# Kernel optimization log

Measured on AMD Instinct MI355X. Metric: run time of the kernel, lower is better.

Reference implementation:

```python
import math
import jax, jax.numpy as jnp
import numpy as np

N, T, F, H = 30000, 4, 128, 8  # num_node, num_type, num_fea, num_head
D = F // H


def setup_inputs() -> dict:
    key = jax.random.key(0)
    k0, k1, k2, k3, k4 = jax.random.split(key, 5)
    feature = jax.random.normal(k0, (N, F), dtype=jnp.float32)
    edge_fea = jax.random.normal(k1, (N, T, F), dtype=jnp.float32)
    node_multi_mask = jax.random.randint(k2, (N,), 0, T)
    # Xavier-uniform-like scale for [*, F, F] projection tables
    xav = math.sqrt(6.0 / (F + F))
    node_proj = jax.random.uniform(k3, (T, F, F), minval=-xav, maxval=xav, dtype=jnp.float32)
    edge_proj = jax.random.uniform(k4, (T * T, F, F), minval=-xav, maxval=xav, dtype=jnp.float32)
    return {
        "feature": feature,
        "edge_fea": edge_fea,
        "node_multi_mask": node_multi_mask,
        "node_proj": node_proj,
        "edge_proj": edge_proj,
    }


def reference(feature, edge_fea, node_multi_mask, node_proj, edge_proj):
    # Type-indexed projections. Instead of gathering per-node [F,F] matrices
    # (which would materialize N*F*F), compute projections for all T source
    # types in one batched einsum, then select each node's type with a gather.
    # node: out[n] = node_proj[mask[n]] @ feature[n]
    node_all = jnp.einsum('tgf,nf->ntg', node_proj, feature)           # [N,T,F]
    node_p = jnp.take_along_axis(node_all, node_multi_mask[:, None, None], axis=1)[:, 0]  # [N,F]
    # edge: out[n,j] = edge_proj[mask[n]*T + j] @ edge_fea[n,j]
    edge_proj_r = edge_proj.reshape(T, T, F, F)                         # [src_type, j, F, F]
    edge_all = jnp.einsum('stgf,ntf->nstg', edge_proj_r, edge_fea)      # [N,T_src,T,F]
    edge_p = jnp.take_along_axis(edge_all, node_multi_mask[:, None, None, None], axis=1)[:, 0]  # [N,T,F]

    # multi-head attention weights
    node_multi_in = node_p.reshape(N, 1, H, D).transpose(0, 2, 1, 3) / math.sqrt(D)  # [N,H,1,D]
    edge_multi_in = edge_p.reshape(N, T, H, D).transpose(0, 2, 3, 1)                  # [N,H,D,T]
    scores = jnp.matmul(node_multi_in, edge_multi_in)                                 # [N,H,1,T]
    # NOTE: original uses nn.Softmax(dim=1) -> softmax over the HEAD axis
    all_r_weight = jax.nn.softmax(scores, axis=1).transpose(0, 3, 1, 2)               # [N,T,H,1]
    return all_r_weight
```

## Files before the change

### kernel.cpp

```cpp
#include <hip/hip_runtime.h>
#include <hip/hip_bf16.h>

#define N_NODES 30000
#define T_TYPES 4
#define F_DIM   128
#define H_HEADS 8

typedef __bf16 bf16x8 __attribute__((ext_vector_type(8)));
typedef __bf16 bf16x4 __attribute__((ext_vector_type(4)));
typedef float  floatx4 __attribute__((ext_vector_type(4)));

#define WS_REORDER 64
#define WS_NPB     480256
#define WS_EPB     611328

__global__ __launch_bounds__(256) void prep_kernel(
    const float* __restrict__ node_proj, const float* __restrict__ edge_proj,
    __bf16* __restrict__ npb, __bf16* __restrict__ epb, int* __restrict__ counts)
{
    int i = blockIdx.x * 256 + threadIdx.x;
    if (i < 4) counts[i] = 0;
    int base = i * 4;
    float4 v;
    __bf16* dst;
    if (base < T_TYPES * F_DIM * F_DIM) {
        v = ((const float4*)node_proj)[i];
        dst = npb + base;
    } else {
        int off = base - T_TYPES * F_DIM * F_DIM;
        v = ((const float4*)edge_proj)[off >> 2];
        dst = epb + off;
    }
    bf16x4 w = { (__bf16)v.x, (__bf16)v.y, (__bf16)v.z, (__bf16)v.w };
    *(bf16x4*)dst = w;
}

__global__ __launch_bounds__(256) void bucket_kernel(
    const int* __restrict__ mask, int* __restrict__ counts, int* __restrict__ reorder)
{
    int n = blockIdx.x * 256 + threadIdx.x;
    int lane = threadIdx.x & 63;
    int t = (n < N_NODES) ? mask[n] : -1;
    #pragma unroll
    for (int tt = 0; tt < T_TYPES; ++tt) {
        unsigned long long b = __ballot(t == tt);
        if (b == 0ull) continue;
        int cnt = __popcll(b);
        int leader = __ffsll((unsigned long long)b) - 1;
        int base = 0;
        if (lane == leader) base = atomicAdd(&counts[tt], cnt);
        base = __shfl(base, leader);
        if (t == tt) {
            int prefix = __popcll(b & ((1ull << lane) - 1ull));
            reorder[tt * N_NODES + base + prefix] = n;
        }
    }
}

__global__ __launch_bounds__(256) void main_kernel(
    const float* __restrict__ feature, const float* __restrict__ edge_fea,
    const int* __restrict__ counts, const int* __restrict__ reorder,
    const __bf16* __restrict__ npb, const __bf16* __restrict__ epb,
    float* __restrict__ out)
{
    const int t = blockIdx.y;
    const int Nt = counts[t];
    const int start = blockIdx.x * 32;
    if (start >= Nt) return;
    const int valid = min(32, Nt - start);

    __shared__ __bf16 Afeat[32][136];
    __shared__ __bf16 Aedge[4][32][136];
    __shared__ float  sc[32][4][H_HEADS];
    __shared__ int    nidx[32];

    const int tid = threadIdx.x;
    if (tid < 32) {
        int s = (tid < valid) ? tid : (valid - 1);
        nidx[tid] = reorder[t * N_NODES + start + s];
    }
    __syncthreads();

    const int colv = tid & 31;
    const int rowg = tid >> 5;
    #pragma unroll
    for (int it = 0; it < 4; ++it) {
        int row = it * 8 + rowg;
        const float* src = feature + (long)nidx[row] * F_DIM;
        float4 v = ((const float4*)src)[colv];
        bf16x4 w = { (__bf16)v.x, (__bf16)v.y, (__bf16)v.z, (__bf16)v.w };
        *(bf16x4*)(&Afeat[row][0] + colv * 4) = w;
    }
    #pragma unroll
    for (int it = 0; it < 16; ++it) {
        int row = it * 8 + rowg;
        int j = row >> 5, r = row & 31;
        const float* src = edge_fea + ((long)nidx[r] * 4 + j) * F_DIM;
        float4 v = ((const float4*)src)[colv];
        bf16x4 w = { (__bf16)v.x, (__bf16)v.y, (__bf16)v.z, (__bf16)v.w };
        *(bf16x4*)(&Aedge[j][r][0] + colv * 4) = w;
    }
    __syncthreads();

    const int lane = tid & 63;
    const int wave = tid >> 6;
    const int ml   = lane & 15;
    const int quad = lane >> 4;
    const int g0   = wave * 32;

    floatx4 accN[2][2] = {};
    {
        const __bf16* a0 = &Afeat[ml][quad * 8];
        const __bf16* a1 = &Afeat[16 + ml][quad * 8];
        const __bf16* b0 = npb + t * (F_DIM * F_DIM) + (g0 + ml) * F_DIM + quad * 8;
        const __bf16* b1 = b0 + 16 * F_DIM;
        #pragma unroll
        for (int k0 = 0; k0 < 128; k0 += 32) {
            bf16x8 A0 = *(const bf16x8*)(a0 + k0);
            bf16x8 A1 = *(const bf16x8*)(a1 + k0);
            bf16x8 B0 = *(const bf16x8*)(b0 + k0);
            bf16x8 B1 = *(const bf16x8*)(b1 + k0);
            accN[0][0] = __builtin_amdgcn_mfma_f32_16x16x32_bf16(A0, B0, accN[0][0], 0, 0, 0);
            accN[0][1] = __builtin_amdgcn_mfma_f32_16x16x32_bf16(A0, B1, accN[0][1], 0, 0, 0);
            accN[1][0] = __builtin_amdgcn_mfma_f32_16x16x32_bf16(A1, B0, accN[1][0], 0, 0, 0);
            accN[1][1] = __builtin_amdgcn_mfma_f32_16x16x32_bf16(A1, B1, accN[1][1], 0, 0, 0);
        }
    }

    #pragma unroll
    for (int j = 0; j < 4; ++j) {
        floatx4 accE[2][2] = {};
        const __bf16* a0 = &Aedge[j][ml][quad * 8];
        const __bf16* a1 = &Aedge[j][16 + ml][quad * 8];
        const __bf16* b0 = epb + (t * 4 + j) * (F_DIM * F_DIM) + (g0 + ml) * F_DIM + quad * 8;
        const __bf16* b1 = b0 + 16 * F_DIM;
        #pragma unroll
        for (int k0 = 0; k0 < 128; k0 += 32) {
            bf16x8 A0 = *(const bf16x8*)(a0 + k0);
            bf16x8 A1 = *(const bf16x8*)(a1 + k0);
            bf16x8 B0 = *(const bf16x8*)(b0 + k0);
            bf16x8 B1 = *(const bf16x8*)(b1 + k0);
            accE[0][0] = __builtin_amdgcn_mfma_f32_16x16x32_bf16(A0, B0, accE[0][0], 0, 0, 0);
            accE[0][1] = __builtin_amdgcn_mfma_f32_16x16x32_bf16(A0, B1, accE[0][1], 0, 0, 0);
            accE[1][0] = __builtin_amdgcn_mfma_f32_16x16x32_bf16(A1, B0, accE[1][0], 0, 0, 0);
            accE[1][1] = __builtin_amdgcn_mfma_f32_16x16x32_bf16(A1, B1, accE[1][1], 0, 0, 0);
        }
        #pragma unroll
        for (int mt = 0; mt < 2; ++mt) {
            #pragma unroll
            for (int nt = 0; nt < 2; ++nt) {
                floatx4 p = accN[mt][nt] * accE[mt][nt];
                #pragma unroll
                for (int s = 1; s < 16; s <<= 1) {
                    p.x += __shfl_xor(p.x, s);
                    p.y += __shfl_xor(p.y, s);
                    p.z += __shfl_xor(p.z, s);
                    p.w += __shfl_xor(p.w, s);
                }
                if (ml == 0) {
                    int h = wave * 2 + nt;
                    int mb = mt * 16 + quad * 4;
                    sc[mb + 0][j][h] = p.x * 0.25f;
                    sc[mb + 1][j][h] = p.y * 0.25f;
                    sc[mb + 2][j][h] = p.z * 0.25f;
                    sc[mb + 3][j][h] = p.w * 0.25f;
                }
            }
        }
    }
    __syncthreads();

    if (tid < 128) {
        int node = tid >> 2, j = tid & 3;
        if (node < valid) {
            float v[8], m = -1e30f;
            #pragma unroll
            for (int h = 0; h < 8; ++h) { v[h] = sc[node][j][h]; m = fmaxf(m, v[h]); }
            float s = 0.f;
            #pragma unroll
            for (int h = 0; h < 8; ++h) { v[h] = __expf(v[h] - m); s += v[h]; }
            float r = 1.0f / s;
            float* o = out + (long)nidx[node] * (T_TYPES * H_HEADS) + j * H_HEADS;
            float4 o0 = { v[0] * r, v[1] * r, v[2] * r, v[3] * r };
            float4 o1 = { v[4] * r, v[5] * r, v[6] * r, v[7] * r };
            ((float4*)o)[0] = o0;
            ((float4*)o)[1] = o1;
        }
    }
}

extern "C" void kernel_launch(void* const* d_in, const int* in_sizes, int n_in,
                              void* d_out, int out_size, void* d_ws, size_t ws_size,
                              hipStream_t stream) {
    const float* feature   = (const float*)d_in[0];
    const float* edge_fea  = (const float*)d_in[1];
    const int*   mask      = (const int*)d_in[2];
    const float* node_proj = (const float*)d_in[3];
    const float* edge_proj = (const float*)d_in[4];
    float* out = (float*)d_out;

    char* ws = (char*)d_ws;
    int*    counts  = (int*)ws;
    int*    reorder = (int*)(ws + WS_REORDER);
    __bf16* npb     = (__bf16*)(ws + WS_NPB);
    __bf16* epb     = (__bf16*)(ws + WS_EPB);

    prep_kernel<<<320, 256, 0, stream>>>(node_proj, edge_proj, npb, epb, counts);
    bucket_kernel<<<(N_NODES + 255) / 256, 256, 0, stream>>>(mask, counts, reorder);
    dim3 grid((N_NODES + 31) / 32, T_TYPES);
    main_kernel<<<grid, 256, 0, stream>>>(feature, edge_fea, counts, reorder, npb, epb, out);
}
```

Baseline: 158.7 us.

## Fuse prep and bucket kernels, shrink edge LDS tile, use DPP reductions

Merges the weight-conversion and bucketing kernels into one launch and zeroes counts with a memset. The main kernel now stages one edge type at a time into a single 32x136 LDS tile, which cuts shared memory and allows a launch-bounds occupancy hint of 7, at the cost of extra barriers and serialized global loads. The grid is flattened with the type interleaved in the low bits, so empty trailing blocks are spread out. The shuffle-xor reductions are replaced with DPP row adds.

```diff
diff --git a/kernel.cpp b/kernel.cpp
--- a/kernel.cpp
+++ b/kernel.cpp
@@ -14,63 +14,77 @@
 #define WS_NPB     480256
 #define WS_EPB     611328
 
-__global__ __launch_bounds__(256) void prep_kernel(
+template <int CTRL>
+static __device__ __forceinline__ float dpp_add(float x) {
+    int xi = __builtin_bit_cast(int, x);
+    int yi = __builtin_amdgcn_update_dpp(xi, xi, CTRL, 0xF, 0xF, true);
+    return x + __builtin_bit_cast(float, yi);
+}
+static __device__ __forceinline__ float sum16(float x) {
+    x = dpp_add<0xB1>(x);
+    x = dpp_add<0x4E>(x);
+    x = dpp_add<0x141>(x);
+    x = dpp_add<0x140>(x);
+    return x;
+}
+
+__global__ __launch_bounds__(256) void prep_bucket_kernel(
     const float* __restrict__ node_proj, const float* __restrict__ edge_proj,
-    __bf16* __restrict__ npb, __bf16* __restrict__ epb, int* __restrict__ counts)
+    const int* __restrict__ mask,
+    __bf16* __restrict__ npb, __bf16* __restrict__ epb,
+    int* __restrict__ counts, int* __restrict__ reorder)
 {
-    int i = blockIdx.x * 256 + threadIdx.x;
-    if (i < 4) counts[i] = 0;
-    int base = i * 4;
-    float4 v;
-    __bf16* dst;
-    if (base < T_TYPES * F_DIM * F_DIM) {
-        v = ((const float4*)node_proj)[i];
-        dst = npb + base;
+    if (blockIdx.x < 320) {
+        int i = blockIdx.x * 256 + threadIdx.x;
+        int base = i * 4;
+        float4 v;
+        __bf16* dst;
+        if (base < T_TYPES * F_DIM * F_DIM) {
+            v = ((const float4*)node_proj)[i];
+            dst = npb + base;
+        } else {
+            int off = base - T_TYPES * F_DIM * F_DIM;
+            v = ((const float4*)edge_proj)[off >> 2];
+            dst = epb + off;
+        }
+        bf16x4 w = { (__bf16)v.x, (__bf16)v.y, (__bf16)v.z, (__bf16)v.w };
+        *(bf16x4*)dst = w;
     } else {
-        int off = base - T_TYPES * F_DIM * F_DIM;
-        v = ((const float4*)edge_proj)[off >> 2];
-        dst = epb + off;
-    }
-    bf16x4 w = { (__bf16)v.x, (__bf16)v.y, (__bf16)v.z, (__bf16)v.w };
-    *(bf16x4*)dst = w;
-}
-
-__global__ __launch_bounds__(256) void bucket_kernel(
-    const int* __restrict__ mask, int* __restrict__ counts, int* __restrict__ reorder)
-{
-    int n = blockIdx.x * 256 + threadIdx.x;
-    int lane = threadIdx.x & 63;
-    int t = (n < N_NODES) ? mask[n] : -1;
-    #pragma unroll
-    for (int tt = 0; tt < T_TYPES; ++tt) {
-        unsigned long long b = __ballot(t == tt);
-        if (b == 0ull) continue;
-        int cnt = __popcll(b);
-        int leader = __ffsll((unsigned long long)b) - 1;
-        int base = 0;
-        if (lane == leader) base = atomicAdd(&counts[tt], cnt);
-        base = __shfl(base, leader);
-        if (t == tt) {
-            int prefix = __popcll(b & ((1ull << lane) - 1ull));
-            reorder[tt * N_NODES + base + prefix] = n;
-        }
-    }
-}
-
-__global__ __launch_bounds__(256) void main_kernel(
+        int n = (blockIdx.x - 320) * 256 + threadIdx.x;
+        int lane = threadIdx.x & 63;
+        int t = (n < N_NODES) ? mask[n] : -1;
+        #pragma unroll
+        for (int tt = 0; tt < T_TYPES; ++tt) {
+            unsigned long long bm = __ballot(t == tt);
+            if (bm == 0ull) continue;
+            int cnt = __popcll(bm);
+            int leader = __ffsll(bm) - 1;
+            int base = 0;
+            if (lane == leader) base = atomicAdd(&counts[tt], cnt);
+            base = __shfl(base, leader);
+            if (t == tt) {
+                int prefix = __popcll(bm & ((1ull << lane) - 1ull));
+                reorder[tt * N_NODES + base + prefix] = n;
+            }
+        }
+    }
+}
+
+__global__ __launch_bounds__(256, 7) void main_kernel(
     const float* __restrict__ feature, const float* __restrict__ edge_fea,
     const int* __restrict__ counts, const int* __restrict__ reorder,
     const __bf16* __restrict__ npb, const __bf16* __restrict__ epb,
     float* __restrict__ out)
 {
-    const int t = blockIdx.y;
+    const int b = blockIdx.x;
+    const int t = b & 3;
+    const int start = (b >> 2) * 32;
     const int Nt = counts[t];
-    const int start = blockIdx.x * 32;
     if (start >= Nt) return;
     const int valid = min(32, Nt - start);
 
     __shared__ __bf16 Afeat[32][136];
-    __shared__ __bf16 Aedge[4][32][136];
+    __shared__ __bf16 Aedge[32][136];
     __shared__ float  sc[32][4][H_HEADS];
     __shared__ int    nidx[32];
 
@@ -86,19 +100,9 @@
     #pragma unroll
     for (int it = 0; it < 4; ++it) {
         int row = it * 8 + rowg;
-        const float* src = feature + (long)nidx[row] * F_DIM;
-        float4 v = ((const float4*)src)[colv];
+        float4 v = ((const float4*)(feature + (long)nidx[row] * F_DIM))[colv];
         bf16x4 w = { (__bf16)v.x, (__bf16)v.y, (__bf16)v.z, (__bf16)v.w };
         *(bf16x4*)(&Afeat[row][0] + colv * 4) = w;
-    }
-    #pragma unroll
-    for (int it = 0; it < 16; ++it) {
-        int row = it * 8 + rowg;
-        int j = row >> 5, r = row & 31;
-        const float* src = edge_fea + ((long)nidx[r] * 4 + j) * F_DIM;
-        float4 v = ((const float4*)src)[colv];
-        bf16x4 w = { (__bf16)v.x, (__bf16)v.y, (__bf16)v.z, (__bf16)v.w };
-        *(bf16x4*)(&Aedge[j][r][0] + colv * 4) = w;
     }
     __syncthreads();
 
@@ -129,34 +133,43 @@
 
     #pragma unroll
     for (int j = 0; j < 4; ++j) {
+        if (j > 0) __syncthreads();
+        #pragma unroll
+        for (int it = 0; it < 4; ++it) {
+            int row = it * 8 + rowg;
+            float4 v = ((const float4*)(edge_fea + ((long)nidx[row] * 4 + j) * F_DIM))[colv];
+            bf16x4 w = { (__bf16)v.x, (__bf16)v.y, (__bf16)v.z, (__bf16)v.w };
+            *(bf16x4*)(&Aedge[row][0] + colv * 4) = w;
+        }
+        __syncthreads();
+
         floatx4 accE[2][2] = {};
-        const __bf16* a0 = &Aedge[j][ml][quad * 8];
-        const __bf16* a1 = &Aedge[j][16 + ml][quad * 8];
-        const __bf16* b0 = epb + (t * 4 + j) * (F_DIM * F_DIM) + (g0 + ml) * F_DIM + quad * 8;
-        const __bf16* b1 = b0 + 16 * F_DIM;
-        #pragma unroll
-        for (int k0 = 0; k0 < 128; k0 += 32) {
-            bf16x8 A0 = *(const bf16x8*)(a0 + k0);
-            bf16x8 A1 = *(const bf16x8*)(a1 + k0);
-            bf16x8 B0 = *(const bf16x8*)(b0 + k0);
-            bf16x8 B1 = *(const bf16x8*)(b1 + k0);
-            accE[0][0] = __builtin_amdgcn_mfma_f32_16x16x32_bf16(A0, B0, accE[0][0], 0, 0, 0);
-            accE[0][1] = __builtin_amdgcn_mfma_f32_16x16x32_bf16(A0, B1, accE[0][1], 0, 0, 0);
-            accE[1][0] = __builtin_amdgcn_mfma_f32_16x16x32_bf16(A1, B0, accE[1][0], 0, 0, 0);
-            accE[1][1] = __builtin_amdgcn_mfma_f32_16x16x32_bf16(A1, B1, accE[1][1], 0, 0, 0);
+        {
+            const __bf16* a0 = &Aedge[ml][quad * 8];
+            const __bf16* a1 = &Aedge[16 + ml][quad * 8];
+            const __bf16* b0 = epb + (t * 4 + j) * (F_DIM * F_DIM) + (g0 + ml) * F_DIM + quad * 8;
+            const __bf16* b1 = b0 + 16 * F_DIM;
+            #pragma unroll
+            for (int k0 = 0; k0 < 128; k0 += 32) {
+                bf16x8 A0 = *(const bf16x8*)(a0 + k0);
+                bf16x8 A1 = *(const bf16x8*)(a1 + k0);
+                bf16x8 B0 = *(const bf16x8*)(b0 + k0);
+                bf16x8 B1 = *(const bf16x8*)(b1 + k0);
+                accE[0][0] = __builtin_amdgcn_mfma_f32_16x16x32_bf16(A0, B0, accE[0][0], 0, 0, 0);
+                accE[0][1] = __builtin_amdgcn_mfma_f32_16x16x32_bf16(A0, B1, accE[0][1], 0, 0, 0);
+                accE[1][0] = __builtin_amdgcn_mfma_f32_16x16x32_bf16(A1, B0, accE[1][0], 0, 0, 0);
+                accE[1][1] = __builtin_amdgcn_mfma_f32_16x16x32_bf16(A1, B1, accE[1][1], 0, 0, 0);
+            }
         }
         #pragma unroll
         for (int mt = 0; mt < 2; ++mt) {
             #pragma unroll
             for (int nt = 0; nt < 2; ++nt) {
                 floatx4 p = accN[mt][nt] * accE[mt][nt];
-                #pragma unroll
-                for (int s = 1; s < 16; s <<= 1) {
-                    p.x += __shfl_xor(p.x, s);
-                    p.y += __shfl_xor(p.y, s);
-                    p.z += __shfl_xor(p.z, s);
-                    p.w += __shfl_xor(p.w, s);
-                }
+                p.x = sum16(p.x);
+                p.y = sum16(p.y);
+                p.z = sum16(p.z);
+                p.w = sum16(p.w);
                 if (ml == 0) {
                     int h = wave * 2 + nt;
                     int mb = mt * 16 + quad * 4;
@@ -205,8 +218,9 @@
     __bf16* npb     = (__bf16*)(ws + WS_NPB);
     __bf16* epb     = (__bf16*)(ws + WS_EPB);
 
-    prep_kernel<<<320, 256, 0, stream>>>(node_proj, edge_proj, npb, epb, counts);
-    bucket_kernel<<<(N_NODES + 255) / 256, 256, 0, stream>>>(mask, counts, reorder);
-    dim3 grid((N_NODES + 31) / 32, T_TYPES);
-    main_kernel<<<grid, 256, 0, stream>>>(feature, edge_fea, counts, reorder, npb, epb, out);
-}
+    hipMemsetAsync(counts, 0, 4 * sizeof(int), stream);
+    prep_bucket_kernel<<<320 + (N_NODES + 255) / 256, 256, 0, stream>>>(
+        node_proj, edge_proj, mask, npb, epb, counts, reorder);
+    int nblk = ((N_NODES + 31) / 32) * T_TYPES;
+    main_kernel<<<nblk, 256, 0, stream>>>(feature, edge_fea, counts, reorder, npb, epb, out);
+}
```

After: 146.2 us. 1.09x faster.
